# Performance work log

Hardware: AMD Instinct MI355X
Metric: run time of the kernel (lower is better)

Reference implementation:

```python
import jax, jax.numpy as jnp
import numpy as np

D_MODEL = 1024
NUM_HEADS = 16
HEAD_DIM = D_MODEL // NUM_HEADS
B, S = 2, 2048


def setup_inputs() -> dict:
    key = jax.random.key(0)
    ks = jax.random.split(key, 6)
    scale = 0.02
    return {
        "x": jax.random.normal(ks[0], (B, S, D_MODEL), dtype=jnp.float32),
        "mask": jax.random.normal(ks[1], (S, S), dtype=jnp.float32),
        "Wqkv": jax.random.normal(ks[2], (D_MODEL, 3 * D_MODEL), dtype=jnp.float32) * scale,
        "bqkv": jax.random.normal(ks[3], (3 * D_MODEL,), dtype=jnp.float32) * scale,
        "Wout": jax.random.normal(ks[4], (D_MODEL, D_MODEL), dtype=jnp.float32) * scale,
        "bout": jax.random.normal(ks[5], (D_MODEL,), dtype=jnp.float32) * scale,
    }


def reference(x, mask, Wqkv, bqkv, Wout, bout):
    b, s, d = x.shape
    h, hd = NUM_HEADS, HEAD_DIM
    qkv = x @ Wqkv + bqkv                              # [b, s, 3d]
    qkv = qkv.reshape(b, s, h, 3 * hd).transpose(0, 2, 1, 3)  # [b, h, s, 3hd]
    q, k, v = jnp.split(qkv, 3, axis=-1)               # each [b, h, s, hd]
    scaled = jnp.einsum("bhqd,bhkd->bhqk", q, k) / jnp.sqrt(jnp.float32(hd))
    scaled = scaled + mask                             # mask [s, s] broadcasts
    attn = jax.nn.softmax(scaled, axis=-1)
    values = jnp.einsum("bhqk,bhkd->bhqd", attn, v)    # [b, h, s, hd]
    values = values.transpose(0, 2, 1, 3).reshape(b, s, d)
    return values @ Wout + bout
```

## Files before the change

### kernel.cpp

```cpp
#include <hip/hip_runtime.h>
#include <hip/hip_bf16.h>

#define D_MODEL 1024
#define NH 16
#define HD 64
#define BATCH 2
#define SEQ 2048
#define M_TOTAL (BATCH*SEQ)

typedef _Float16 f16;
typedef _Float16 half8 __attribute__((ext_vector_type(8)));
typedef _Float16 half4v __attribute__((ext_vector_type(4)));
typedef float floatx4 __attribute__((ext_vector_type(4)));

#if __has_builtin(__builtin_amdgcn_exp2f)
#define EXP2(x) __builtin_amdgcn_exp2f(x)
#else
#define EXP2(x) __expf(0.6931471805599453f * (x))
#endif

__device__ inline void gload_lds16(const void* g, void* l) {
    __builtin_amdgcn_global_load_lds(
        (const __attribute__((address_space(1))) unsigned int*)g,
        (__attribute__((address_space(3))) unsigned int*)l, 16, 0, 0);
}

__device__ void trans_body(const float* __restrict__ src, f16* __restrict__ dst,
                           int R, int C, int bx, int by) {
    __shared__ float tile[32][33];
    int tx = threadIdx.x & 31;
    int ty = threadIdx.x >> 5;
    int c0 = bx * 32;
    int r0 = by * 32;
    for (int yy = 0; yy < 32; yy += 8)
        tile[ty + yy][tx] = src[(long)(r0 + ty + yy) * C + c0 + tx];
    __syncthreads();
    for (int yy = 0; yy < 32; yy += 8)
        dst[(long)(c0 + ty + yy) * R + r0 + tx] = (f16)tile[tx][ty + yy];
}

__global__ __launch_bounds__(256) void prep(
    const float* __restrict__ x, f16* __restrict__ xh,
    const float* __restrict__ Wqkv, f16* __restrict__ WqkvT,
    const float* __restrict__ Wout, f16* __restrict__ WoutT,
    const float* __restrict__ mask, f16* __restrict__ E)
{
    int bid = blockIdx.x;
    if (bid < 1024) {
        int i = bid * 256 + threadIdx.x;
        #pragma unroll
        for (int it = 0; it < 4; ++it, i += 262144) {
            float4 v = ((const float4*)x)[i];
            half4v o = { (f16)v.x, (f16)v.y, (f16)v.z, (f16)v.w };
            *(half4v*)(xh + (long)i * 4) = o;
        }
    } else if (bid < 1024 + 3072) {
        int t = bid - 1024;
        trans_body(Wqkv, WqkvT, 1024, 3072, t % 96, t / 96);
    } else if (bid < 5120) {
        int t = bid - 4096;
        trans_body(Wout, WoutT, 1024, 1024, t % 32, t / 32);
    } else {
        int i = (bid - 5120) * 256 + threadIdx.x;
        float4 v = ((const float4*)mask)[i];
        const float L2E = 1.44269504f;
        half4v o = { (f16)(v.x * L2E), (f16)(v.y * L2E), (f16)(v.z * L2E), (f16)(v.w * L2E) };
        *(half4v*)(E + (long)i * 4) = o;
    }
}

__global__ void l2scale_cvt(const float* __restrict__ src, f16* __restrict__ dst, int n4) {
    int i = blockIdx.x * blockDim.x + threadIdx.x;
    if (i < n4) {
        float4 v = ((const float4*)src)[i];
        const float L2E = 1.44269504f;
        half4v o = { (f16)(v.x * L2E), (f16)(v.y * L2E), (f16)(v.z * L2E), (f16)(v.w * L2E) };
        *(half4v*)(dst + (long)i * 4) = o;
    }
}

template<int MODE, int TN>
__global__ __launch_bounds__(256) void gemm_mfma(
    const f16* __restrict__ A, const f16* __restrict__ BT,
    const float* __restrict__ bias,
    f16* __restrict__ Qh, f16* __restrict__ Kh, f16* __restrict__ Vtg,
    float* __restrict__ out, int Kdim)
{
    constexpr int NF = TN / 32;
    __shared__ f16 Ah[2][128 * 32];
    __shared__ f16 Bh[2][TN * 32];
    int tid  = threadIdx.x;
    int wid  = tid >> 6;
    int lane = tid & 63;
    int quad = lane >> 4;
    int l16  = lane & 15;
    int m0 = blockIdx.y * 128;
    int n0 = blockIdx.x * TN;
    int mrow = (wid >> 1) * 64;
    int ncol = (wid & 1) * (TN / 2);
    int srow = lane >> 2;
    int gchunk = (lane & 3) ^ (srow & 3);
    int sw = (quad ^ (l16 & 3)) * 8;

    floatx4 acc[4][NF];
    #pragma unroll
    for (int mb = 0; mb < 4; mb++)
        #pragma unroll
        for (int nb = 0; nb < NF; nb++) acc[mb][nb] = (floatx4){0.f, 0.f, 0.f, 0.f};

    const f16* Abase = A + (long)m0 * Kdim;
    const f16* Bbase = BT + (long)n0 * Kdim;

    auto stage = [&](int buf, int k0) {
        #pragma unroll
        for (int j = 0; j < 2; j++) {
            int r = wid * 32 + j * 16 + srow;
            gload_lds16(Abase + (long)r * Kdim + k0 + gchunk * 8, &Ah[buf][(wid * 32 + j * 16) * 32]);
        }
        if (TN == 128) {
            #pragma unroll
            for (int j = 0; j < 2; j++) {
                int r = wid * 32 + j * 16 + srow;
                gload_lds16(Bbase + (long)r * Kdim + k0 + gchunk * 8, &Bh[buf][(wid * 32 + j * 16) * 32]);
            }
        } else {
            int r = wid * 16 + srow;
            gload_lds16(Bbase + (long)r * Kdim + k0 + gchunk * 8, &Bh[buf][(wid * 16) * 32]);
        }
    };

    stage(0, 0);
    __syncthreads();
    int cur = 0;
    for (int k0 = 0; k0 < Kdim; k0 += 32) {
        if (k0 + 32 < Kdim) stage(cur ^ 1, k0 + 32);
        half8 af[4];
        #pragma unroll
        for (int mb = 0; mb < 4; mb++)
            af[mb] = *(const half8*)&Ah[cur][(mrow + mb * 16 + l16) * 32 + sw];
        #pragma unroll
        for (int nb = 0; nb < NF; nb++) {
            half8 bf = *(const half8*)&Bh[cur][(ncol + nb * 16 + l16) * 32 + sw];
            #pragma unroll
            for (int mb = 0; mb < 4; mb++)
                acc[mb][nb] = __builtin_amdgcn_mfma_f32_16x16x32_f16(af[mb], bf, acc[mb][nb], 0, 0, 0);
        }
        __syncthreads();
        cur ^= 1;
    }

    #pragma unroll
    for (int nb = 0; nb < NF; nb++) {
        int n = n0 + ncol + nb * 16 + l16;
        float bv = bias[n];
        int head = 0, t = 0, d = 0;
        if (MODE == 0) { head = n / 192; int rem = n % 192; t = rem / 64; d = rem % 64; }
        #pragma unroll
        for (int mb = 0; mb < 4; mb++) {
            int mbase = m0 + mrow + mb * 16 + quad * 4;
            if (MODE == 0) {
                int b = mbase >> 11;
                int s = mbase & 2047;
                long bh = b * NH + head;
                if (t == 2) {
                    half4v pack;
                    #pragma unroll
                    for (int r = 0; r < 4; r++) pack[r] = (f16)(acc[mb][nb][r] + bv);
                    *(half4v*)&Vtg[(bh * HD + d) * SEQ + s] = pack;
                } else if (t == 0) {
                    #pragma unroll
                    for (int r = 0; r < 4; r++)
                        Qh[(bh * SEQ + s + r) * HD + d] = (f16)((acc[mb][nb][r] + bv) * 0.18033688f);
                } else {
                    #pragma unroll
                    for (int r = 0; r < 4; r++)
                        Kh[(bh * SEQ + s + r) * HD + d] = (f16)(acc[mb][nb][r] + bv);
                }
            } else {
                #pragma unroll
                for (int r = 0; r < 4; r++)
                    out[(long)(mbase + r) * D_MODEL + n] = acc[mb][nb][r] + bv;
            }
        }
    }
}

__global__ __launch_bounds__(512) void attn(
    const f16* __restrict__ Qh, const f16* __restrict__ Kh, const f16* __restrict__ Vtg,
    const f16* __restrict__ E, f16* __restrict__ valh)
{
    extern __shared__ f16 sm[];
    f16* Kt0 = sm;
    f16* Kt1 = sm + 4096;
    f16* Vt0 = sm + 8192;
    f16* Vt1 = sm + 12288;
    f16* Plb = sm + 16384;
    int tid  = threadIdx.x;
    int wid  = tid >> 6;
    int lane = tid & 63;
    int quad = lane >> 4;
    int l16  = lane & 15;
    int qg = wid & 3;
    int kg = wid >> 2;

    int id   = blockIdx.y * 16 + blockIdx.x;
    int xcd  = id & 7;
    int slot = id >> 3;
    int bh   = ((xcd & 3) << 3) | (slot >> 3);
    int qx   = ((xcd >> 2) << 3) | (slot & 7);
    int b  = bh >> 4;
    int h  = bh & 15;
    int qblk = qx * 128;
    int q0 = qblk + qg * 32;

    int grow = lane >> 3;
    int gchunk = (lane & 7) ^ (grow & 7);
    int sw0 = ((quad)     ^ (l16 & 7)) * 8;
    int sw1 = ((quad + 4) ^ (l16 & 7)) * 8;

    const f16* Qbase = Qh + ((long)bh * SEQ + q0) * HD;
    half8 qf[2][2];
    #pragma unroll
    for (int m = 0; m < 2; m++)
        #pragma unroll
        for (int c = 0; c < 2; c++)
            qf[m][c] = *(const half8*)&Qbase[(long)(m * 16 + l16) * HD + c * 32 + quad * 8];

    half8 onesv;
    #pragma unroll
    for (int j = 0; j < 8; j++) onesv[j] = (f16)1.0f;

    floatx4 Of[2][4];
    floatx4 ssum[2];
    #pragma unroll
    for (int m = 0; m < 2; m++) {
        ssum[m] = (floatx4){0.f, 0.f, 0.f, 0.f};
        #pragma unroll
        for (int nb = 0; nb < 4; nb++) Of[m][nb] = (floatx4){0.f, 0.f, 0.f, 0.f};
    }

    const f16* Kb = Kh + (long)bh * SEQ * HD;
    const f16* Vb = Vtg + (long)bh * HD * SEQ;
    const f16* Eb = E + (long)qblk * SEQ;

    int stile = wid >> 1;
    f16* sdst = (stile == 0) ? Kt0 : (stile == 1) ? Kt1 : (stile == 2) ? Vt0 : Vt1;
    bool sK = (stile < 2);
    int skodd = stile & 1;

    f16* Kt = kg ? Kt1 : Kt0;
    f16* Vt = kg ? Vt1 : Vt0;
    f16* Pl = Plb + wid * (32 * 68);

    for (int t = 0; t < 16; ++t) {
        if (t) __syncthreads();
        {
            int kk = (2 * t + skodd) * 64;
            #pragma unroll
            for (int j = 0; j < 4; j++) {
                int r = (wid & 1) * 32 + j * 8 + grow;
                const f16* src = sK ? (Kb + (long)(kk + r) * HD + gchunk * 8)
                                    : (Vb + (long)r * SEQ + kk + gchunk * 8);
                gload_lds16(src, &sdst[((wid & 1) * 32 + j * 8) * 64]);
            }
        }
        __syncthreads();

        int k0 = (2 * t + kg) * 64;

        f16 ef[2][4][4];
        #pragma unroll
        for (int m = 0; m < 2; m++)
            #pragma unroll
            for (int r = 0; r < 4; r++) {
                const f16* Erow = Eb + (long)(qg * 32 + m * 16 + quad * 4 + r) * SEQ + k0 + l16;
                #pragma unroll
                for (int kb = 0; kb < 4; kb++) ef[m][r][kb] = Erow[kb * 16];
            }

        floatx4 sc[2][4];
        __builtin_amdgcn_s_setprio(1);
        #pragma unroll
        for (int kb = 0; kb < 4; kb++) {
            half8 kf0 = *(const half8*)&Kt[(kb * 16 + l16) * 64 + sw0];
            half8 kf1 = *(const half8*)&Kt[(kb * 16 + l16) * 64 + sw1];
            #pragma unroll
            for (int m = 0; m < 2; m++) {
                floatx4 sacc = (floatx4){0.f, 0.f, 0.f, 0.f};
                sacc = __builtin_amdgcn_mfma_f32_16x16x32_f16(qf[m][0], kf0, sacc, 0, 0, 0);
                sacc = __builtin_amdgcn_mfma_f32_16x16x32_f16(qf[m][1], kf1, sacc, 0, 0, 0);
                sc[m][kb] = sacc;
            }
        }
        __builtin_amdgcn_s_setprio(0);

        #pragma unroll
        for (int m = 0; m < 2; m++)
            #pragma unroll
            for (int kb = 0; kb < 4; kb++)
                #pragma unroll
                for (int r = 0; r < 4; r++) {
                    float p = EXP2(sc[m][kb][r] + (float)ef[m][r][kb]);
                    Pl[(m * 16 + quad * 4 + r) * 68 + kb * 16 + l16] = (f16)p;
                }

        half8 pf[2][2];
        #pragma unroll
        for (int m = 0; m < 2; m++)
            #pragma unroll
            for (int c = 0; c < 2; c++)
                pf[m][c] = *(const half8*)&Pl[(m * 16 + l16) * 68 + c * 32 + quad * 8];

        __builtin_amdgcn_s_setprio(1);
        #pragma unroll
        for (int m = 0; m < 2; m++) {
            ssum[m] = __builtin_amdgcn_mfma_f32_16x16x32_f16(pf[m][0], onesv, ssum[m], 0, 0, 0);
            ssum[m] = __builtin_amdgcn_mfma_f32_16x16x32_f16(pf[m][1], onesv, ssum[m], 0, 0, 0);
        }
        #pragma unroll
        for (int nb = 0; nb < 4; nb++) {
            half8 vf0 = *(const half8*)&Vt[(nb * 16 + l16) * 64 + sw0];
            half8 vf1 = *(const half8*)&Vt[(nb * 16 + l16) * 64 + sw1];
            #pragma unroll
            for (int m = 0; m < 2; m++) {
                Of[m][nb] = __builtin_amdgcn_mfma_f32_16x16x32_f16(pf[m][0], vf0, Of[m][nb], 0, 0, 0);
                Of[m][nb] = __builtin_amdgcn_mfma_f32_16x16x32_f16(pf[m][1], vf1, Of[m][nb], 0, 0, 0);
            }
        }
        __builtin_amdgcn_s_setprio(0);
    }

    __syncthreads();
    float* xch = (float*)sm;
    float* p = xch + (long)(qg * 64 + lane) * 48;
    if (kg == 1) {
        #pragma unroll
        for (int m = 0; m < 2; m++)
            #pragma unroll
            for (int nb = 0; nb < 4; nb++)
                *(floatx4*)(p + (m * 4 + nb) * 4) = Of[m][nb];
        *(floatx4*)(p + 32) = ssum[0];
        *(floatx4*)(p + 40) = ssum[1];
    }
    __syncthreads();
    if (kg == 0) {
        #pragma unroll
        for (int m = 0; m < 2; m++) {
            #pragma unroll
            for (int nb = 0; nb < 4; nb++)
                Of[m][nb] += *(const floatx4*)(p + (m * 4 + nb) * 4);
            ssum[m] += *(const floatx4*)(p + 32 + m * 8);
        }
        float rinv[2][4];
        #pragma unroll
        for (int m = 0; m < 2; m++)
            #pragma unroll
            for (int r = 0; r < 4; r++) rinv[m][r] = 1.f / ssum[m][r];

        #pragma unroll
        for (int m = 0; m < 2; m++)
            #pragma unroll
            for (int nb = 0; nb < 4; nb++)
                #pragma unroll
                for (int r = 0; r < 4; r++) {
                    int q = q0 + m * 16 + quad * 4 + r;
                    int d = nb * 16 + l16;
                    valh[((long)(b * SEQ + q)) * D_MODEL + h * HD + d] = (f16)(Of[m][nb][r] * rinv[m][r]);
                }
    }
}

extern "C" void kernel_launch(void* const* d_in, const int* in_sizes, int n_in,
                              void* d_out, int out_size, void* d_ws, size_t ws_size,
                              hipStream_t stream) {
    const float* x    = (const float*)d_in[0];
    const float* mask = (const float*)d_in[1];
    const float* Wqkv = (const float*)d_in[2];
    const float* bqkv = (const float*)d_in[3];
    const float* Wout = (const float*)d_in[4];
    const float* bout = (const float*)d_in[5];
    float* out = (float*)d_out;

    char* ws = (char*)d_ws;
    f16* xh    = (f16*)(ws + 0);
    f16* WqkvT = (f16*)(ws + 8388608);
    f16* WoutT = (f16*)(ws + 14680064);
    f16* Qh    = (f16*)(ws + 16777216);
    f16* Kh    = (f16*)(ws + 25165824);
    f16* Vtg   = (f16*)(ws + 33554432);
    f16* valh  = (f16*)(ws + 41943040);

    bool sepE = (ws_size >= 58720256);
    f16* E = sepE ? (f16*)(ws + 50331648)
                  : (f16*)(ws + 0);

    if (sepE) {
        prep<<<9216, 256, 0, stream>>>(x, xh, Wqkv, WqkvT, Wout, WoutT, mask, E);
        gemm_mfma<0, 128><<<dim3(24, 32), 256, 0, stream>>>(xh, WqkvT, bqkv, Qh, Kh, Vtg, nullptr, 1024);
    } else {
        prep<<<5120, 256, 0, stream>>>(x, xh, Wqkv, WqkvT, Wout, WoutT, mask, E);
        gemm_mfma<0, 128><<<dim3(24, 32), 256, 0, stream>>>(xh, WqkvT, bqkv, Qh, Kh, Vtg, nullptr, 1024);
        l2scale_cvt<<<4096, 256, 0, stream>>>(mask, E, SEQ * SEQ / 4);
    }
    attn<<<dim3(16, 32), 512, 67584, stream>>>(Qh, Kh, Vtg, E, valh);
    gemm_mfma<1, 64><<<dim3(16, 32), 256, 0, stream>>>(valh, WoutT, bout, nullptr, nullptr, nullptr, out, 1024);
}
```

Before: 252.7 us.

## Double-buffer K/V tiles in attention and split each tile's keys across key-groups

The attention loop now walks 64-key tiles with double-buffered K/V LDS staging, so the next tile is prefetched while the current one is computed, and there is one barrier per iteration. Before, each key-group took its own 64-key tile with a load-then-wait pattern and two barriers per iteration. Each key-group now handles half of the keys of a shared tile: 32 keys against all 64 V dims, using the swizzled column halves. This shrinks the per-wave P buffer and the dynamic LDS footprint, and it pads the exchange buffer to an odd stride to reduce bank conflicts. The risks are smaller per-iteration MFMA batches and misaligned 16-byte LDS accesses in the exchange area.

Result: faster. 227.1 us (-10.1%).

```diff
diff --git a/kernel.cpp b/kernel.cpp
--- a/kernel.cpp
+++ b/kernel.cpp
@@ -190,8 +190,8 @@
     const f16* __restrict__ E, f16* __restrict__ valh)
 {
     extern __shared__ f16 sm[];
-    f16* Kt0 = sm;
-    f16* Kt1 = sm + 4096;
+    f16* Kl0 = sm;
+    f16* Kl1 = sm + 4096;
     f16* Vt0 = sm + 8192;
     f16* Vt1 = sm + 12288;
     f16* Plb = sm + 16384;
@@ -213,10 +213,11 @@
     int qblk = qx * 128;
     int q0 = qblk + qg * 32;
 
-    int grow = lane >> 3;
-    int gchunk = (lane & 7) ^ (grow & 7);
+    int wrow = wid * 8 + (lane >> 3);
+    int kchunk = (lane & 7) ^ (wrow & 7);
     int sw0 = ((quad)     ^ (l16 & 7)) * 8;
     int sw1 = ((quad + 4) ^ (l16 & 7)) * 8;
+    int swv = kg ? sw1 : sw0;
 
     const f16* Qbase = Qh + ((long)bh * SEQ + q0) * HD;
     half8 qf[2][2];
@@ -243,45 +244,39 @@
     const f16* Vb = Vtg + (long)bh * HD * SEQ;
     const f16* Eb = E + (long)qblk * SEQ;
 
-    int stile = wid >> 1;
-    f16* sdst = (stile == 0) ? Kt0 : (stile == 1) ? Kt1 : (stile == 2) ? Vt0 : Vt1;
-    bool sK = (stile < 2);
-    int skodd = stile & 1;
-
-    f16* Kt = kg ? Kt1 : Kt0;
-    f16* Vt = kg ? Vt1 : Vt0;
-    f16* Pl = Plb + wid * (32 * 68);
-
-    for (int t = 0; t < 16; ++t) {
-        if (t) __syncthreads();
-        {
-            int kk = (2 * t + skodd) * 64;
-            #pragma unroll
-            for (int j = 0; j < 4; j++) {
-                int r = (wid & 1) * 32 + j * 8 + grow;
-                const f16* src = sK ? (Kb + (long)(kk + r) * HD + gchunk * 8)
-                                    : (Vb + (long)r * SEQ + kk + gchunk * 8);
-                gload_lds16(src, &sdst[((wid & 1) * 32 + j * 8) * 64]);
+    f16* Pl = Plb + wid * (32 * 36);
+
+    auto stage = [&](f16* Kd, f16* Vd, int k0) {
+        gload_lds16(Kb + (long)(k0 + wrow) * HD + kchunk * 8, &Kd[(wid * 8) * 64]);
+        gload_lds16(Vb + (long)wrow * SEQ + k0 + kchunk * 8, &Vd[(wid * 8) * 64]);
+    };
+
+    stage(Kl0, Vt0, 0);
+    __syncthreads();
+
+    for (int t = 0; t < 32; ++t) {
+        int buf = t & 1;
+        f16* Kt = buf ? Kl1 : Kl0;
+        f16* Vt = buf ? Vt1 : Vt0;
+        int k0 = t * 64;
+        if (t + 1 < 32) stage(buf ? Kl0 : Kl1, buf ? Vt0 : Vt1, k0 + 64);
+
+        f16 ef[2][2][4];
+        #pragma unroll
+        for (int m = 0; m < 2; m++)
+            #pragma unroll
+            for (int r = 0; r < 4; r++) {
+                const f16* Erow = Eb + (long)(qg * 32 + m * 16 + quad * 4 + r) * SEQ
+                                     + k0 + kg * 32 + l16;
+                #pragma unroll
+                for (int kbl = 0; kbl < 2; kbl++) ef[m][kbl][r] = Erow[kbl * 16];
             }
-        }
-        __syncthreads();
-
-        int k0 = (2 * t + kg) * 64;
-
-        f16 ef[2][4][4];
-        #pragma unroll
-        for (int m = 0; m < 2; m++)
-            #pragma unroll
-            for (int r = 0; r < 4; r++) {
-                const f16* Erow = Eb + (long)(qg * 32 + m * 16 + quad * 4 + r) * SEQ + k0 + l16;
-                #pragma unroll
-                for (int kb = 0; kb < 4; kb++) ef[m][r][kb] = Erow[kb * 16];
-            }
-
-        floatx4 sc[2][4];
+
+        floatx4 sc[2][2];
         __builtin_amdgcn_s_setprio(1);
         #pragma unroll
-        for (int kb = 0; kb < 4; kb++) {
+        for (int kbl = 0; kbl < 2; kbl++) {
+            int kb = kg * 2 + kbl;
             half8 kf0 = *(const half8*)&Kt[(kb * 16 + l16) * 64 + sw0];
             half8 kf1 = *(const half8*)&Kt[(kb * 16 + l16) * 64 + sw1];
             #pragma unroll
@@ -289,7 +284,7 @@
                 floatx4 sacc = (floatx4){0.f, 0.f, 0.f, 0.f};
                 sacc = __builtin_amdgcn_mfma_f32_16x16x32_f16(qf[m][0], kf0, sacc, 0, 0, 0);
                 sacc = __builtin_amdgcn_mfma_f32_16x16x32_f16(qf[m][1], kf1, sacc, 0, 0, 0);
-                sc[m][kb] = sacc;
+                sc[m][kbl] = sacc;
             }
         }
         __builtin_amdgcn_s_setprio(0);
@@ -297,42 +292,36 @@
         #pragma unroll
         for (int m = 0; m < 2; m++)
             #pragma unroll
-            for (int kb = 0; kb < 4; kb++)
+            for (int kbl = 0; kbl < 2; kbl++)
                 #pragma unroll
                 for (int r = 0; r < 4; r++) {
-                    float p = EXP2(sc[m][kb][r] + (float)ef[m][r][kb]);
-                    Pl[(m * 16 + quad * 4 + r) * 68 + kb * 16 + l16] = (f16)p;
+                    float p = EXP2(sc[m][kbl][r] + (float)ef[m][kbl][r]);
+                    Pl[(m * 16 + quad * 4 + r) * 36 + kbl * 16 + l16] = (f16)p;
                 }
 
-        half8 pf[2][2];
-        #pragma unroll
-        for (int m = 0; m < 2; m++)
-            #pragma unroll
-            for (int c = 0; c < 2; c++)
-                pf[m][c] = *(const half8*)&Pl[(m * 16 + l16) * 68 + c * 32 + quad * 8];
+        half8 pf[2];
+        #pragma unroll
+        for (int m = 0; m < 2; m++)
+            pf[m] = *(const half8*)&Pl[(m * 16 + l16) * 36 + quad * 8];
 
         __builtin_amdgcn_s_setprio(1);
         #pragma unroll
-        for (int m = 0; m < 2; m++) {
-            ssum[m] = __builtin_amdgcn_mfma_f32_16x16x32_f16(pf[m][0], onesv, ssum[m], 0, 0, 0);
-            ssum[m] = __builtin_amdgcn_mfma_f32_16x16x32_f16(pf[m][1], onesv, ssum[m], 0, 0, 0);
-        }
+        for (int m = 0; m < 2; m++)
+            ssum[m] = __builtin_amdgcn_mfma_f32_16x16x32_f16(pf[m], onesv, ssum[m], 0, 0, 0);
         #pragma unroll
         for (int nb = 0; nb < 4; nb++) {
-            half8 vf0 = *(const half8*)&Vt[(nb * 16 + l16) * 64 + sw0];
-            half8 vf1 = *(const half8*)&Vt[(nb * 16 + l16) * 64 + sw1];
-            #pragma unroll
-            for (int m = 0; m < 2; m++) {
-                Of[m][nb] = __builtin_amdgcn_mfma_f32_16x16x32_f16(pf[m][0], vf0, Of[m][nb], 0, 0, 0);
-                Of[m][nb] = __builtin_amdgcn_mfma_f32_16x16x32_f16(pf[m][1], vf1, Of[m][nb], 0, 0, 0);
-            }
+            half8 vf = *(const half8*)&Vt[(nb * 16 + l16) * 64 + swv];
+            #pragma unroll
+            for (int m = 0; m < 2; m++)
+                Of[m][nb] = __builtin_amdgcn_mfma_f32_16x16x32_f16(pf[m], vf, Of[m][nb], 0, 0, 0);
         }
         __builtin_amdgcn_s_setprio(0);
-    }
-
-    __syncthreads();
+
+        __syncthreads();
+    }
+
     float* xch = (float*)sm;
-    float* p = xch + (long)(qg * 64 + lane) * 48;
+    float* p = xch + (long)(qg * 64 + lane) * 41;
     if (kg == 1) {
         #pragma unroll
         for (int m = 0; m < 2; m++)
@@ -340,7 +329,7 @@
             for (int nb = 0; nb < 4; nb++)
                 *(floatx4*)(p + (m * 4 + nb) * 4) = Of[m][nb];
         *(floatx4*)(p + 32) = ssum[0];
-        *(floatx4*)(p + 40) = ssum[1];
+        *(floatx4*)(p + 36) = ssum[1];
     }
     __syncthreads();
     if (kg == 0) {
@@ -349,7 +338,7 @@
             #pragma unroll
             for (int nb = 0; nb < 4; nb++)
                 Of[m][nb] += *(const floatx4*)(p + (m * 4 + nb) * 4);
-            ssum[m] += *(const floatx4*)(p + 32 + m * 8);
+            ssum[m] += *(const floatx4*)(p + 32 + m * 4);
         }
         float rinv[2][4];
         #pragma unroll
@@ -402,6 +391,6 @@
         gemm_mfma<0, 128><<<dim3(24, 32), 256, 0, stream>>>(xh, WqkvT, bqkv, Qh, Kh, Vtg, nullptr, 1024);
         l2scale_cvt<<<4096, 256, 0, stream>>>(mask, E, SEQ * SEQ / 4);
     }
-    attn<<<dim3(16, 32), 512, 67584, stream>>>(Qh, Kh, Vtg, E, valh);
+    attn<<<dim3(16, 32), 512, 51200, stream>>>(Qh, Kh, Vtg, E, valh);
     gemm_mfma<1, 64><<<dim3(16, 32), 256, 0, stream>>>(valh, WoutT, bout, nullptr, nullptr, nullptr, out, 1024);
 }
```
